# Kernel tuning notes

Measured on AMD Instinct MI355X. Metric: run time of the kernel, lower is better.

## Reference

```python
import jax, jax.numpy as jnp
import numpy as np

NUM_LAYERS = 4

def setup_inputs() -> dict:
    key = jax.random.key(0)
    x = jax.random.normal(key, (4000000, 9), dtype=jnp.float32)
    return {"x": x}

def reference(x) -> jnp.ndarray:
    # reshape to batched 3x3 matrices
    xm = x.reshape(-1, 3, 3)
    # Frobenius norm per matrix, keepdims for broadcast
    norm = jnp.sqrt(jnp.sum(xm * xm, axis=(1, 2), keepdims=True))
    Q = xm / norm
    for _ in range(NUM_LAYERS):
        # N = Q^T Q  (b33)
        N = jnp.einsum('bji,bjk->bik', Q, Q)
        P = 0.5 * jnp.einsum('bij,bjk->bik', Q, N)
        Q = 2.0 * Q + jnp.einsum('bij,bjk->bik', P, N) - 3.0 * P
    return Q.reshape(x.shape)
```

## Files before the change

### kernel.cpp

```cpp
#include <hip/hip_runtime.h>


#define NLAYERS 4

__global__ __launch_bounds__(256) void
proj_kernel(const float* __restrict__ x, float* __restrict__ out) {
    __shared__ float lds[256 * 9];
    const int tid = threadIdx.x;
    const long long mbase = (long long)blockIdx.x * 256;

    const float4* __restrict__ gin = (const float4*)(x + mbase * 9);
    float4* lds4 = (float4*)lds;
    lds4[tid]       = gin[tid];
    lds4[tid + 256] = gin[tid + 256];
    if (tid < 64) lds4[tid + 512] = gin[tid + 512];
    __syncthreads();

    float q[9];
#pragma unroll
    for (int k = 0; k < 9; ++k) q[k] = lds[tid * 9 + k];
    __syncthreads();

    float s = 0.f;
#pragma unroll
    for (int k = 0; k < 9; ++k) s += q[k] * q[k];
    const float inv = rsqrtf(s);
#pragma unroll
    for (int k = 0; k < 9; ++k) q[k] *= inv;

#pragma unroll
    for (int layer = 0; layer < NLAYERS; ++layer) {
        float n00 = q[0]*q[0] + q[3]*q[3] + q[6]*q[6];
        float n01 = q[0]*q[1] + q[3]*q[4] + q[6]*q[7];
        float n02 = q[0]*q[2] + q[3]*q[5] + q[6]*q[8];
        float n11 = q[1]*q[1] + q[4]*q[4] + q[7]*q[7];
        float n12 = q[1]*q[2] + q[4]*q[5] + q[7]*q[8];
        float n22 = q[2]*q[2] + q[5]*q[5] + q[8]*q[8];
        float N[3][3] = {{n00, n01, n02}, {n01, n11, n12}, {n02, n12, n22}};

        float p[9];
#pragma unroll
        for (int i = 0; i < 3; ++i)
#pragma unroll
            for (int j = 0; j < 3; ++j)
                p[3*i+j] = 0.5f * (q[3*i+0]*N[0][j] + q[3*i+1]*N[1][j] + q[3*i+2]*N[2][j]);

        float r[9];
#pragma unroll
        for (int i = 0; i < 3; ++i)
#pragma unroll
            for (int j = 0; j < 3; ++j)
                r[3*i+j] = p[3*i+0]*N[0][j] + p[3*i+1]*N[1][j] + p[3*i+2]*N[2][j];

#pragma unroll
        for (int k = 0; k < 9; ++k) q[k] = 2.0f*q[k] + r[k] - 3.0f*p[k];
    }

#pragma unroll
    for (int k = 0; k < 9; ++k) lds[tid * 9 + k] = q[k];
    __syncthreads();

    float4* __restrict__ gout = (float4*)(out + mbase * 9);
    gout[tid]       = lds4[tid];
    gout[tid + 256] = lds4[tid + 256];
    if (tid < 64) gout[tid + 512] = lds4[tid + 512];
}

extern "C" void kernel_launch(void* const* d_in, const int* in_sizes, int n_in,
                              void* d_out, int out_size, void* d_ws, size_t ws_size,
                              hipStream_t stream) {
    const float* x = (const float*)d_in[0];
    float* out = (float*)d_out;
    const int nmat = in_sizes[0] / 9;
    const int blocks = nmat / 256;
    proj_kernel<<<blocks, 256, 0, stream>>>(x, out);
}
```

Before: 249.1 us.

## Fold layer update into single Q*M product, split LDS buffers, nontemporal stores

Rewrites each layer algebraically as Q_new = Q·M, where M = 2I - 1.5N + 0.5N² is built from the symmetric N with FMAs. This replaces the two 3x3 matrix products and the elementwise combine with one symmetric 3x3 build plus one matrix product. It also gives input and output separate LDS buffers so the middle __syncthreads can be dropped, and writes output with nontemporal stores. The costs are doubled LDS use per block, which may lower occupancy, and slightly different floating-point rounding. The kernel is likely memory-bound, so the ALU savings may matter less than the store and LDS changes.

```diff
diff --git a/kernel.cpp b/kernel.cpp
--- a/kernel.cpp
+++ b/kernel.cpp
@@ -3,67 +3,80 @@
 
 #define NLAYERS 4
 
+typedef float v4f __attribute__((ext_vector_type(4)));
+
 __global__ __launch_bounds__(256) void
 proj_kernel(const float* __restrict__ x, float* __restrict__ out) {
-    __shared__ float lds[256 * 9];
+    __shared__ float lin[256 * 9];
+    __shared__ float lout[256 * 9];
     const int tid = threadIdx.x;
     const long long mbase = (long long)blockIdx.x * 256;
 
-    const float4* __restrict__ gin = (const float4*)(x + mbase * 9);
-    float4* lds4 = (float4*)lds;
-    lds4[tid]       = gin[tid];
-    lds4[tid + 256] = gin[tid + 256];
-    if (tid < 64) lds4[tid + 512] = gin[tid + 512];
+    const v4f* __restrict__ gin = (const v4f*)(x + mbase * 9);
+    v4f* lin4 = (v4f*)lin;
+    lin4[tid]       = gin[tid];
+    lin4[tid + 256] = gin[tid + 256];
+    if (tid < 64) lin4[tid + 512] = gin[tid + 512];
     __syncthreads();
 
     float q[9];
 #pragma unroll
-    for (int k = 0; k < 9; ++k) q[k] = lds[tid * 9 + k];
-    __syncthreads();
+    for (int k = 0; k < 9; ++k) q[k] = lin[tid * 9 + k];
 
     float s = 0.f;
 #pragma unroll
-    for (int k = 0; k < 9; ++k) s += q[k] * q[k];
+    for (int k = 0; k < 9; ++k) s = __builtin_fmaf(q[k], q[k], s);
     const float inv = rsqrtf(s);
 #pragma unroll
     for (int k = 0; k < 9; ++k) q[k] *= inv;
 
 #pragma unroll
     for (int layer = 0; layer < NLAYERS; ++layer) {
-        float n00 = q[0]*q[0] + q[3]*q[3] + q[6]*q[6];
-        float n01 = q[0]*q[1] + q[3]*q[4] + q[6]*q[7];
-        float n02 = q[0]*q[2] + q[3]*q[5] + q[6]*q[8];
-        float n11 = q[1]*q[1] + q[4]*q[4] + q[7]*q[7];
-        float n12 = q[1]*q[2] + q[4]*q[5] + q[7]*q[8];
-        float n22 = q[2]*q[2] + q[5]*q[5] + q[8]*q[8];
-        float N[3][3] = {{n00, n01, n02}, {n01, n11, n12}, {n02, n12, n22}};
+        const float n00 = q[0]*q[0] + q[3]*q[3] + q[6]*q[6];
+        const float n01 = q[0]*q[1] + q[3]*q[4] + q[6]*q[7];
+        const float n02 = q[0]*q[2] + q[3]*q[5] + q[6]*q[8];
+        const float n11 = q[1]*q[1] + q[4]*q[4] + q[7]*q[7];
+        const float n12 = q[1]*q[2] + q[4]*q[5] + q[7]*q[8];
+        const float n22 = q[2]*q[2] + q[5]*q[5] + q[8]*q[8];
 
-        float p[9];
+        const float a00 = __builtin_fmaf(0.5f, n00, -1.5f);
+        const float a11 = __builtin_fmaf(0.5f, n11, -1.5f);
+        const float a22 = __builtin_fmaf(0.5f, n22, -1.5f);
+        const float a01 = 0.5f * n01;
+        const float a02 = 0.5f * n02;
+        const float a12 = 0.5f * n12;
+
+        const float m00 = __builtin_fmaf(a00,n00, __builtin_fmaf(a01,n01, __builtin_fmaf(a02,n02, 2.0f)));
+        const float m01 = __builtin_fmaf(a00,n01, __builtin_fmaf(a01,n11, a02*n12));
+        const float m02 = __builtin_fmaf(a00,n02, __builtin_fmaf(a01,n12, a02*n22));
+        const float m11 = __builtin_fmaf(a01,n01, __builtin_fmaf(a11,n11, __builtin_fmaf(a12,n12, 2.0f)));
+        const float m12 = __builtin_fmaf(a01,n02, __builtin_fmaf(a11,n12, a12*n22));
+        const float m22 = __builtin_fmaf(a02,n02, __builtin_fmaf(a12,n12, __builtin_fmaf(a22,n22, 2.0f)));
+
+        const float M[3][3] = {{m00, m01, m02}, {m01, m11, m12}, {m02, m12, m22}};
+
+        float qn[9];
 #pragma unroll
         for (int i = 0; i < 3; ++i)
 #pragma unroll
             for (int j = 0; j < 3; ++j)
-                p[3*i+j] = 0.5f * (q[3*i+0]*N[0][j] + q[3*i+1]*N[1][j] + q[3*i+2]*N[2][j]);
-
-        float r[9];
+                qn[3*i+j] = __builtin_fmaf(q[3*i+0], M[0][j],
+                            __builtin_fmaf(q[3*i+1], M[1][j],
+                                           q[3*i+2] * M[2][j]));
 #pragma unroll
-        for (int i = 0; i < 3; ++i)
-#pragma unroll
-            for (int j = 0; j < 3; ++j)
-                r[3*i+j] = p[3*i+0]*N[0][j] + p[3*i+1]*N[1][j] + p[3*i+2]*N[2][j];
-
-#pragma unroll
-        for (int k = 0; k < 9; ++k) q[k] = 2.0f*q[k] + r[k] - 3.0f*p[k];
+        for (int k = 0; k < 9; ++k) q[k] = qn[k];
     }
 
 #pragma unroll
-    for (int k = 0; k < 9; ++k) lds[tid * 9 + k] = q[k];
+    for (int k = 0; k < 9; ++k) lout[tid * 9 + k] = q[k];
     __syncthreads();
 
-    float4* __restrict__ gout = (float4*)(out + mbase * 9);
-    gout[tid]       = lds4[tid];
-    gout[tid + 256] = lds4[tid + 256];
-    if (tid < 64) gout[tid + 512] = lds4[tid + 512];
+    v4f* __restrict__ gout = (v4f*)(out + mbase * 9);
+    const v4f* lout4 = (const v4f*)lout;
+    __builtin_nontemporal_store(lout4[tid],       gout + tid);
+    __builtin_nontemporal_store(lout4[tid + 256], gout + tid + 256);
+    if (tid < 64)
+        __builtin_nontemporal_store(lout4[tid + 512], gout + tid + 512);
 }
 
 extern "C" void kernel_launch(void* const* d_in, const int* in_sizes, int n_in,
```

Result: no change. 245.9 us (-1.3%).
